# Kernel tuning notes

Measured on AMD Instinct MI355X. Metric: run time of the kernel, lower is better.

Reference implementation:

```python
import jax, jax.numpy as jnp
import numpy as np

B, D, H, NG = 8192, 2048, 2048, 7  # batch, input_size, hidden_size, num gate networks


def setup_inputs() -> dict:
    key = jax.random.key(0)
    ks = jax.random.split(key, 7)
    hx = jax.random.normal(ks[0], (B, D), dtype=jnp.float32)
    cx1 = jax.random.normal(ks[1], (B, H), dtype=jnp.float32)
    cx2 = jax.random.normal(ks[2], (B, H), dtype=jnp.float32)
    tj = jax.random.uniform(ks[3], (B, 1), dtype=jnp.float32)
    dt = jax.random.uniform(ks[4], (B, 1), dtype=jnp.float32)
    # fused weights for the 7 gate/decay networks, order: i1,i2,f1,f2,o,z,d
    W = jax.random.normal(ks[5], (D, NG * H), dtype=jnp.float32) * (1.0 / np.sqrt(D))
    b = jax.random.normal(ks[6], (NG * H,), dtype=jnp.float32) * 0.01
    return {"hx": hx, "cx1": cx1, "cx2": cx2, "tj": tj, "dt": dt, "W": W, "b": b}


def reference(hx, cx1, cx2, tj, dt, W, b):
    # One fused GEMM for all 7 gate networks, then split.
    g = hx @ W + b  # [B, 7H]
    i1, i2, f1, f2, o, z_raw, d_raw = [g[:, k * H:(k + 1) * H] for k in range(NG)]
    sig = jax.nn.sigmoid
    i1, i2, f1, f2, o = sig(i1), sig(i2), sig(f1), sig(f2), sig(o)
    z = jnp.tanh(z_raw)                 # Tanh(LC_z(hx)) as in forward
    decay = jax.nn.softplus(d_raw)      # Decay_network: positive decay coeff
    cy1 = f1 * cx1 + i1 * z             # fast cell state
    cy2 = f2 * cx2 + i2 * z             # asymptotic cell state
    t = tj + dt
    # continuous-time decay: c(t) = cy2 + (cy1 - cy2) * exp(-decay * (t - tj))
    c_t = cy2 + (cy1 - cy2) * jnp.exp(-decay * (t - tj))
    h_t = o * jnp.tanh(c_t)             # get_h(t)
    return jnp.stack([cy1, cy2, h_t])   # [3, B, H]
```

## Files before the change

### kernel.cpp

```cpp
#include <hip/hip_runtime.h>
#include <hip/hip_bf16.h>
#include <stdint.h>


#define B_SZ 8192
#define D_SZ 2048
#define H_SZ 2048
#define NG   7
#define NW   (NG * H_SZ)
#define BM   256
#define BK   64
#define NKT  (D_SZ / BK)
#define NBX  (B_SZ / BM)
#define NNB  (H_SZ / 32)

#define ATILE 32768
#define BTILE 28672
#define WB_BYTES   ((size_t)NNB * NKT * BTILE)
#define AB_OFF     WB_BYTES
#define AB_BYTES   ((size_t)NBX * NKT * ATILE)
#define WS_NEEDED  (WB_BYTES + AB_BYTES)

typedef __attribute__((ext_vector_type(8))) short bf16x8;
typedef __attribute__((ext_vector_type(4))) float f32x4;

__device__ __forceinline__ uint32_t cvtpk(float lo, float hi) {
    uint32_t r;
    asm("v_cvt_pk_bf16_f32 %0, %1, %2" : "=v"(r) : "v"(lo), "v"(hi));
    return r;
}
__device__ __forceinline__ void glds16(const void* g, void* l) {
    __builtin_amdgcn_global_load_lds(
        (const __attribute__((address_space(1))) uint32_t*)g,
        (__attribute__((address_space(3))) uint32_t*)l, 16, 0, 0);
}
__device__ __forceinline__ float sigmoidf_(float x) {
    return 1.0f / (1.0f + __expf(-x));
}
__device__ __forceinline__ float tanhf_(float x) {
    float ax = fabsf(x);
    float e = __expf(2.0f * ax);
    float t = 1.0f - 2.0f / (e + 1.0f);
    return copysignf(t, x);
}
__device__ __forceinline__ float softplusf_(float x) {
    return (x > 30.0f) ? x : __logf(1.0f + __expf(x));
}

__global__ __launch_bounds__(512) void conv_a(const float* __restrict__ hx,
                                              char* __restrict__ ai)
{
    const int bx = blockIdx.x >> 5;
    const int kt = blockIdx.x & 31;
    char* dst = ai + (size_t)(bx * NKT + kt) * ATILE;
    #pragma unroll
    for (int i = 0; i < 4; ++i) {
        int d = threadIdx.x + i * 512;
        int r = d >> 3, kq = d & 7;
        int koct = kq ^ ((r >> 1) & 3);
        const float* s = hx + (size_t)(bx * BM + r) * D_SZ + kt * BK + koct * 8;
        f32x4 a = *(const f32x4*)s;
        f32x4 b = *(const f32x4*)(s + 4);
        uint4 o;
        o.x = cvtpk(a[0], a[1]); o.y = cvtpk(a[2], a[3]);
        o.z = cvtpk(b[0], b[1]); o.w = cvtpk(b[2], b[3]);
        *(uint4*)(dst + d * 16) = o;
    }
}

__global__ __launch_bounds__(448) void conv_b(const float* __restrict__ W,
                                              char* __restrict__ bi)
{
    const int nb = blockIdx.x >> 5;
    const int kt = blockIdx.x & 31;
    char* dst = bi + (size_t)(nb * NKT + kt) * BTILE;
    const int cc = threadIdx.x % 224;
    const int kh = threadIdx.x / 224;
    const int q  = cc >> 4;
    const int gate = (q < 7) ? q : q - 7;
    const int hsub = ((q < 7) ? 0 : 16) + (cc & 15);
    const int n = gate * H_SZ + nb * 32 + hsub;
    #pragma unroll
    for (int i = 0; i < 4; ++i) {
        int kq = kh * 4 + i;
        int koct = kq ^ ((cc >> 1) & 3);
        const float* s = W + (size_t)(kt * BK + koct * 8) * NW + n;
        float w0 = s[0];
        float w1 = s[(size_t)NW];
        float w2 = s[(size_t)2 * NW];
        float w3 = s[(size_t)3 * NW];
        float w4 = s[(size_t)4 * NW];
        float w5 = s[(size_t)5 * NW];
        float w6 = s[(size_t)6 * NW];
        float w7 = s[(size_t)7 * NW];
        uint4 o;
        o.x = cvtpk(w0, w1); o.y = cvtpk(w2, w3);
        o.z = cvtpk(w4, w5); o.w = cvtpk(w6, w7);
        *(uint4*)(dst + cc * 128 + kq * 16) = o;
    }
}

#define MFMA_ __builtin_amdgcn_mfma_f32_16x16x32_bf16
#define SB0 __builtin_amdgcn_sched_barrier(0)
#define DSR(DST, BASE, OFF) \
    asm volatile("ds_read_b128 %0, %1 offset:" #OFF : "=v"(DST) : "v"(BASE));

__global__ __launch_bounds__(512, 2) void lstm_gemm(
    const char* __restrict__ bi, const char* __restrict__ ai,
    const float* __restrict__ cx1, const float* __restrict__ cx2,
    const float* __restrict__ dt, const float* __restrict__ bias,
    float* __restrict__ out)
{
    __shared__ char smem[2 * 61440];

    const int tid  = threadIdx.x;
    const int lane = tid & 63;
    const int wid  = tid >> 6;
    const int wm4  = wid >> 1;
    const int wn2  = wid & 1;
    const int l15  = lane & 15;
    const int lg   = lane >> 4;

    const int b0  = blockIdx.x;
    const int swz = (b0 & 7) * 256 + (b0 >> 3);
    const int bx  = swz >> 6;
    const int nb  = swz & 63;

    const int xch = lg ^ ((l15 >> 1) & 3);
    const uint32_t aA0 = (uint32_t)(uintptr_t)smem + wm4 * 8192 + l15 * 128 + xch * 16;
    const uint32_t aA1 = aA0 + 61440;
    const uint32_t aB0 = (uint32_t)(uintptr_t)smem + 32768 + wn2 * 14336 + l15 * 128 + xch * 16;
    const uint32_t aB1 = aB0 + 61440;

    char* dstA0 = smem + (wid << 12);
    char* dstA1 = dstA0 + 61440;
    char* dstB0 = smem + 32768 + wid * 3584;
    char* dstB1 = dstB0 + 61440;

    const char* qa = ai + (size_t)bx * (NKT * ATILE) + (wid << 12) + (lane << 4);
    const char* qb = bi + (size_t)nb * (NKT * BTILE) + wid * 3584 + (lane << 4);

    f32x4 acc[NG][4];
    #pragma unroll
    for (int g = 0; g < NG; ++g)
        #pragma unroll
        for (int mf = 0; mf < 4; ++mf)
            acc[g][mf] = (f32x4){0.f, 0.f, 0.f, 0.f};

    bf16x8 fA[4][2], fB0[2], fB1[2];

    #define RD_A(AA) \
        DSR(fA[0][0], AA, 0)    DSR(fA[0][1], AA, 64) \
        DSR(fA[1][0], AA, 2048) DSR(fA[1][1], AA, 2112) \
        DSR(fA[2][0], AA, 4096) DSR(fA[2][1], AA, 4160) \
        DSR(fA[3][0], AA, 6144) DSR(fA[3][1], AA, 6208)

    #define RD_B2(AB, O0, O1, O2, O3) \
        DSR(fB0[0], AB, O0) DSR(fB0[1], AB, O1) \
        DSR(fB1[0], AB, O2) DSR(fB1[1], AB, O3)

    #define PH_SYNC \
        SB0; __builtin_amdgcn_s_barrier(); \
        asm volatile("s_waitcnt lgkmcnt(0)" ::: "memory"); SB0;

    #define CL16(NA, NX) \
        __builtin_amdgcn_s_setprio(1); \
        _Pragma("unroll") \
        for (int mf_ = 0; mf_ < 4; ++mf_) { \
            acc[NA][mf_] = MFMA_(fA[mf_][0], fB0[0], acc[NA][mf_], 0, 0, 0); \
            acc[NA][mf_] = MFMA_(fA[mf_][1], fB0[1], acc[NA][mf_], 0, 0, 0); \
        } \
        _Pragma("unroll") \
        for (int mf_ = 0; mf_ < 4; ++mf_) { \
            acc[NX][mf_] = MFMA_(fA[mf_][0], fB1[0], acc[NX][mf_], 0, 0, 0); \
            acc[NX][mf_] = MFMA_(fA[mf_][1], fB1[1], acc[NX][mf_], 0, 0, 0); \
        } \
        __builtin_amdgcn_s_setprio(0); SB0;

    #define STG_A(NB_) do { \
        glds16(psA, dstA##NB_);            glds16(psA + 1024, dstA##NB_ + 1024); \
        glds16(psA + 2048, dstA##NB_ + 2048); glds16(psA + 3072, dstA##NB_ + 3072); \
        psA += ATILE; } while (0)

    #define STG_B(NB_) do { \
        glds16(psB, dstB##NB_);            glds16(psB + 1024, dstB##NB_ + 1024); \
        glds16(psB + 2048, dstB##NB_ + 2048); \
        if (lane < 32) glds16(psB + 3072, dstB##NB_ + 3072); \
        psB += BTILE; } while (0)

    #define TILE(B_, N_, STG) do { \
         \
        RD_A(aA##B_) \
        RD_B2(aB##B_, 0, 64, 2048, 2112) \
        if (STG) STG_A(N_); \
        PH_SYNC \
        CL16(0, 1) \
        __builtin_amdgcn_s_barrier(); \
         \
        RD_B2(aB##B_, 4096, 4160, 6144, 6208) \
        if (STG) STG_B(N_); \
        PH_SYNC \
        CL16(2, 3) \
        __builtin_amdgcn_s_barrier(); \
         \
        RD_B2(aB##B_, 8192, 8256, 10240, 10304) \
        PH_SYNC \
        CL16(4, 5) \
        __builtin_amdgcn_s_barrier(); \
         \
        DSR(fB0[0], aB##B_, 12288) DSR(fB0[1], aB##B_, 12352) \
        PH_SYNC \
        __builtin_amdgcn_s_setprio(1); \
        _Pragma("unroll") \
        for (int mf_ = 0; mf_ < 4; ++mf_) { \
            acc[6][mf_] = MFMA_(fA[mf_][0], fB0[0], acc[6][mf_], 0, 0, 0); \
            acc[6][mf_] = MFMA_(fA[mf_][1], fB0[1], acc[6][mf_], 0, 0, 0); \
        } \
        __builtin_amdgcn_s_setprio(0); SB0; \
        asm volatile("s_waitcnt vmcnt(0)" ::: "memory"); \
        __builtin_amdgcn_s_barrier(); \
        SB0; \
    } while (0)

    glds16(qa, dstA0);        glds16(qa + 1024, dstA0 + 1024);
    glds16(qa + 2048, dstA0 + 2048); glds16(qa + 3072, dstA0 + 3072);
    glds16(qb, dstB0);        glds16(qb + 1024, dstB0 + 1024);
    glds16(qb + 2048, dstB0 + 2048);
    if (lane < 32) glds16(qb + 3072, dstB0 + 3072);
    const char* psA = qa + ATILE;
    const char* psB = qb + BTILE;
    asm volatile("s_waitcnt vmcnt(0)" ::: "memory");
    __builtin_amdgcn_s_barrier();
    SB0;

    #pragma unroll 1
    for (int it = 0; it < 16; ++it) {
        TILE(0, 1, 1);
        TILE(1, 0, (it < 15));
    }

    const size_t BH = (size_t)B_SZ * H_SZ;
    const int h = nb * 32 + wn2 * 16 + l15;
    float bj[NG];
    #pragma unroll
    for (int g = 0; g < NG; ++g) bj[g] = bias[g * H_SZ + h];

    #pragma unroll
    for (int mf = 0; mf < 4; ++mf) {
        #pragma unroll
        for (int r = 0; r < 4; ++r) {
            int row = bx * BM + wm4 * 64 + mf * 16 + lg * 4 + r;
            float dtv = dt[row];
            float i1 = sigmoidf_(acc[0][mf][r] + bj[0]);
            float i2 = sigmoidf_(acc[1][mf][r] + bj[1]);
            float f1 = sigmoidf_(acc[2][mf][r] + bj[2]);
            float f2 = sigmoidf_(acc[3][mf][r] + bj[3]);
            float o  = sigmoidf_(acc[4][mf][r] + bj[4]);
            float z  = tanhf_(acc[5][mf][r] + bj[5]);
            float dec = softplusf_(acc[6][mf][r] + bj[6]);
            size_t idx = (size_t)row * H_SZ + h;
            float c1 = cx1[idx], c2 = cx2[idx];
            float cy1 = f1 * c1 + i1 * z;
            float cy2 = f2 * c2 + i2 * z;
            float ct  = cy2 + (cy1 - cy2) * __expf(-dec * dtv);
            float ht  = o * tanhf_(ct);
            out[idx]          = cy1;
            out[BH + idx]     = cy2;
            out[2 * BH + idx] = ht;
        }
    }
}

#define BN_  32
#define NTH  512
#define LDP  40
#define NKST 64
__global__ __launch_bounds__(NTH, 2) void lstm_f32(
    const float* __restrict__ hx, const float* __restrict__ cx1,
    const float* __restrict__ cx2, const float* __restrict__ dt,
    const float* __restrict__ W, const float* __restrict__ bias,
    float* __restrict__ out)
{
    __shared__ ushort sA[BM * LDP];
    __shared__ ushort sB[NG * BN_ * LDP];

    const int tid = threadIdx.x;
    const int nwg = gridDim.x;
    const int cpx = nwg >> 3;
    const int b0  = blockIdx.x;
    const int swz = (b0 & 7) * cpx + (b0 >> 3);
    const int bx  = swz & 31;
    const int by  = swz >> 5;
    const int gm0 = bx * BM;
    const int n0  = by * BN_;

    const int lane = tid & 63;
    const int wid  = tid >> 6;
    const int wm   = wid >> 1;
    const int wn   = wid & 1;
    const int l15  = lane & 15;
    const int lg   = lane >> 4;

    const int ar0 = tid >> 2,          aq0 = tid & 3;
    const int ar1 = (tid + 512) >> 2,  aq1 = tid & 3;
    const bool hasB = (tid < 448);
    const int bg  = tid >> 6;
    const int bkq = (tid >> 3) & 7;
    const int bnq = tid & 7;

    f32x4 pa[4];
    f32x4 pb[4];

    auto issue_loads = [&](int K0) {
        {
            const float* p = hx + (size_t)(gm0 + ar0) * D_SZ + K0 + aq0 * 8;
            pa[0] = *(const f32x4*)(p);
            pa[1] = *(const f32x4*)(p + 4);
        }
        {
            const float* p = hx + (size_t)(gm0 + ar1) * D_SZ + K0 + aq1 * 8;
            pa[2] = *(const f32x4*)(p);
            pa[3] = *(const f32x4*)(p + 4);
        }
        if (hasB) {
            const float* p = W + (size_t)(K0 + bkq * 4) * NW + bg * H_SZ + n0 + bnq * 4;
            pb[0] = *(const f32x4*)(p);
            pb[1] = *(const f32x4*)(p + NW);
            pb[2] = *(const f32x4*)(p + 2 * NW);
            pb[3] = *(const f32x4*)(p + 3 * NW);
        }
    };

    auto store_lds = [&]() {
        {
            uint4 u;
            u.x = cvtpk(pa[0][0], pa[0][1]); u.y = cvtpk(pa[0][2], pa[0][3]);
            u.z = cvtpk(pa[1][0], pa[1][1]); u.w = cvtpk(pa[1][2], pa[1][3]);
            *(uint4*)(&sA[ar0 * LDP + aq0 * 8]) = u;
        }
        {
            uint4 u;
            u.x = cvtpk(pa[2][0], pa[2][1]); u.y = cvtpk(pa[2][2], pa[2][3]);
            u.z = cvtpk(pa[3][0], pa[3][1]); u.w = cvtpk(pa[3][2], pa[3][3]);
            *(uint4*)(&sA[ar1 * LDP + aq1 * 8]) = u;
        }
        if (hasB) {
            #pragma unroll
            for (int jj = 0; jj < 4; ++jj) {
                uint2 v;
                v.x = cvtpk(pb[0][jj], pb[1][jj]);
                v.y = cvtpk(pb[2][jj], pb[3][jj]);
                *(uint2*)(&sB[(bg * BN_ + bnq * 4 + jj) * LDP + bkq * 4]) = v;
            }
        }
    };

    f32x4 acc[NG][4];
    #pragma unroll
    for (int g = 0; g < NG; ++g)
        #pragma unroll
        for (int mf = 0; mf < 4; ++mf)
            acc[g][mf] = (f32x4){0.f, 0.f, 0.f, 0.f};

    int aoff[4];
    #pragma unroll
    for (int mf = 0; mf < 4; ++mf)
        aoff[mf] = (wm * 64 + mf * 16 + l15) * LDP + lg * 8;
    int boff[NG];
    #pragma unroll
    for (int g = 0; g < NG; ++g)
        boff[g] = (g * BN_ + wn * 16 + l15) * LDP + lg * 8;

    issue_loads(0);
    for (int kk = 0; kk < NKST; ++kk) {
        store_lds();
        __syncthreads();
        if (kk + 1 < NKST) issue_loads((kk + 1) * 32);

        bf16x8 af[4];
        #pragma unroll
        for (int mf = 0; mf < 4; ++mf)
            af[mf] = *(const bf16x8*)(&sA[aoff[mf]]);
        #pragma unroll
        for (int g = 0; g < NG; ++g) {
            bf16x8 bfr = *(const bf16x8*)(&sB[boff[g]]);
            #pragma unroll
            for (int mf = 0; mf < 4; ++mf)
                acc[g][mf] = __builtin_amdgcn_mfma_f32_16x16x32_bf16(
                    af[mf], bfr, acc[g][mf], 0, 0, 0);
        }
        __syncthreads();
    }

    const size_t BH = (size_t)B_SZ * H_SZ;
    const int j = n0 + wn * 16 + l15;
    float bj[NG];
    #pragma unroll
    for (int g = 0; g < NG; ++g) bj[g] = bias[g * H_SZ + j];

    #pragma unroll
    for (int mf = 0; mf < 4; ++mf) {
        #pragma unroll
        for (int r = 0; r < 4; ++r) {
            int row = gm0 + wm * 64 + mf * 16 + lg * 4 + r;
            float dtv = dt[row];
            float i1 = sigmoidf_(acc[0][mf][r] + bj[0]);
            float i2 = sigmoidf_(acc[1][mf][r] + bj[1]);
            float f1 = sigmoidf_(acc[2][mf][r] + bj[2]);
            float f2 = sigmoidf_(acc[3][mf][r] + bj[3]);
            float o  = sigmoidf_(acc[4][mf][r] + bj[4]);
            float z  = tanhf_(acc[5][mf][r] + bj[5]);
            float dec = softplusf_(acc[6][mf][r] + bj[6]);
            size_t idx = (size_t)row * H_SZ + j;
            float c1 = cx1[idx], c2 = cx2[idx];
            float cy1 = f1 * c1 + i1 * z;
            float cy2 = f2 * c2 + i2 * z;
            float ct  = cy2 + (cy1 - cy2) * __expf(-dec * dtv);
            float ht  = o * tanhf_(ct);
            out[idx]          = cy1;
            out[BH + idx]     = cy2;
            out[2 * BH + idx] = ht;
        }
    }
}

extern "C" void kernel_launch(void* const* d_in, const int* in_sizes, int n_in,
                              void* d_out, int out_size, void* d_ws, size_t ws_size,
                              hipStream_t stream) {
    const float* hx  = (const float*)d_in[0];
    const float* cx1 = (const float*)d_in[1];
    const float* cx2 = (const float*)d_in[2];
    const float* dt  = (const float*)d_in[4];
    const float* W   = (const float*)d_in[5];
    const float* b   = (const float*)d_in[6];
    float* out = (float*)d_out;

    if (ws_size >= WS_NEEDED) {
        char* bimg = (char*)d_ws;
        char* aimg = (char*)d_ws + AB_OFF;
        conv_b<<<dim3(NNB * NKT), dim3(448), 0, stream>>>(W, bimg);
        conv_a<<<dim3(NBX * NKT), dim3(512), 0, stream>>>(hx, aimg);
        lstm_gemm<<<dim3(NBX * NNB), dim3(512), 0, stream>>>(
            bimg, aimg, cx1, cx2, dt, b, out);
    } else {
        lstm_f32<<<dim3(NBX * NNB / 2), dim3(NTH), 0, stream>>>(
            hx, cx1, cx2, dt, W, b, out);
    }
}
```

Baseline: 602.5 us.

## Split K tiles into 32-wide halves with finer-grained async LDS pipelining

Repacks the bf16 A and B images into two 32-wide K halves (64-byte rows) so each MFMA consumes one full fragment, and restructures the main loop to issue the loads for each half separately. Partial vmcnt waits replace the full drain at the end of each tile, so global-to-LDS copies overlap more with compute. The block-to-tile mapping is also changed so that pairs of N blocks share an A tile, aiming for better L2 reuse. The tradeoff is more barriers per tile and more intricate vmcnt bookkeeping, which risks races if the counts are wrong.

```diff
diff --git a/kernel.cpp b/kernel.cpp
--- a/kernel.cpp
+++ b/kernel.cpp
@@ -9,8 +9,7 @@
 #define NG   7
 #define NW   (NG * H_SZ)
 #define BM   256
-#define BK   64
-#define NKT  (D_SZ / BK)
+#define NKT  32
 #define NBX  (B_SZ / BM)
 #define NNB  (H_SZ / 32)
 
@@ -47,25 +46,22 @@
     return (x > 30.0f) ? x : __logf(1.0f + __expf(x));
 }
 
-__global__ __launch_bounds__(512) void conv_a(const float* __restrict__ hx,
-                                              char* __restrict__ ai)
+__global__ __launch_bounds__(1024) void conv_a(const float* __restrict__ hx,
+                                               char* __restrict__ ai)
 {
-    const int bx = blockIdx.x >> 5;
-    const int kt = blockIdx.x & 31;
-    char* dst = ai + (size_t)(bx * NKT + kt) * ATILE;
-    #pragma unroll
-    for (int i = 0; i < 4; ++i) {
-        int d = threadIdx.x + i * 512;
-        int r = d >> 3, kq = d & 7;
-        int koct = kq ^ ((r >> 1) & 3);
-        const float* s = hx + (size_t)(bx * BM + r) * D_SZ + kt * BK + koct * 8;
-        f32x4 a = *(const f32x4*)s;
-        f32x4 b = *(const f32x4*)(s + 4);
-        uint4 o;
-        o.x = cvtpk(a[0], a[1]); o.y = cvtpk(a[2], a[3]);
-        o.z = cvtpk(b[0], b[1]); o.w = cvtpk(b[2], b[3]);
-        *(uint4*)(dst + d * 16) = o;
-    }
+    const int bx = blockIdx.x >> 6;
+    const int ks = blockIdx.x & 63;
+    const int u  = threadIdx.x;
+    const int r  = u >> 2;
+    const int pc = u & 3;
+    const int koct = pc ^ ((r >> 1) & 3);
+    const float* src = hx + (size_t)(bx * BM + r) * D_SZ + ks * 32 + koct * 8;
+    f32x4 a = *(const f32x4*)(src);
+    f32x4 b = *(const f32x4*)(src + 4);
+    uint4 o;
+    o.x = cvtpk(a[0], a[1]); o.y = cvtpk(a[2], a[3]);
+    o.z = cvtpk(b[0], b[1]); o.w = cvtpk(b[2], b[3]);
+    *(uint4*)(ai + (size_t)blockIdx.x * 16384 + u * 16) = o;
 }
 
 __global__ __launch_bounds__(448) void conv_b(const float* __restrict__ W,
@@ -73,18 +69,18 @@
 {
     const int nb = blockIdx.x >> 5;
     const int kt = blockIdx.x & 31;
-    char* dst = bi + (size_t)(nb * NKT + kt) * BTILE;
+    char* dst = bi + (size_t)blockIdx.x * BTILE;
     const int cc = threadIdx.x % 224;
     const int kh = threadIdx.x / 224;
     const int q  = cc >> 4;
     const int gate = (q < 7) ? q : q - 7;
     const int hsub = ((q < 7) ? 0 : 16) + (cc & 15);
-    const int n = gate * H_SZ + nb * 32 + hsub;
-    #pragma unroll
-    for (int i = 0; i < 4; ++i) {
-        int kq = kh * 4 + i;
-        int koct = kq ^ ((cc >> 1) & 3);
-        const float* s = W + (size_t)(kt * BK + koct * 8) * NW + n;
+    const int n  = gate * H_SZ + nb * 32 + hsub;
+    const int xb = (cc >> 1) & 3;
+    #pragma unroll
+    for (int pc = 0; pc < 4; ++pc) {
+        const int k = kt * 64 + kh * 32 + (pc ^ xb) * 8;
+        const float* s = W + (size_t)k * NW + n;
         float w0 = s[0];
         float w1 = s[(size_t)NW];
         float w2 = s[(size_t)2 * NW];
@@ -96,7 +92,7 @@
         uint4 o;
         o.x = cvtpk(w0, w1); o.y = cvtpk(w2, w3);
         o.z = cvtpk(w4, w5); o.w = cvtpk(w6, w7);
-        *(uint4*)(dst + cc * 128 + kq * 16) = o;
+        *(uint4*)(dst + kh * 14336 + cc * 64 + pc * 16) = o;
     }
 }
 
@@ -123,22 +119,24 @@
 
     const int b0  = blockIdx.x;
     const int swz = (b0 & 7) * 256 + (b0 >> 3);
-    const int bx  = swz >> 6;
-    const int nb  = swz & 63;
+    const int nb2 = swz >> 6;
+    const int rem = swz & 63;
+    const int bx  = rem >> 1;
+    const int nb  = nb2 * 2 + (rem & 1);
 
     const int xch = lg ^ ((l15 >> 1) & 3);
-    const uint32_t aA0 = (uint32_t)(uintptr_t)smem + wm4 * 8192 + l15 * 128 + xch * 16;
-    const uint32_t aA1 = aA0 + 61440;
-    const uint32_t aB0 = (uint32_t)(uintptr_t)smem + 32768 + wn2 * 14336 + l15 * 128 + xch * 16;
-    const uint32_t aB1 = aB0 + 61440;
-
-    char* dstA0 = smem + (wid << 12);
-    char* dstA1 = dstA0 + 61440;
-    char* dstB0 = smem + 32768 + wid * 3584;
-    char* dstB1 = dstB0 + 61440;
-
-    const char* qa = ai + (size_t)bx * (NKT * ATILE) + (wid << 12) + (lane << 4);
-    const char* qb = bi + (size_t)nb * (NKT * BTILE) + wid * 3584 + (lane << 4);
+    const uint32_t aAb = (uint32_t)(uintptr_t)smem
+                       + (wm4 * 64 + l15) * 64 + xch * 16;
+    const uint32_t aBb = (uint32_t)(uintptr_t)smem + 32768
+                       + (wn2 * 112 + l15) * 64 + xch * 16;
+    const uint32_t aA0 = aAb, aA1 = aAb + 61440;
+    const uint32_t aB0 = aBb, aB1 = aBb + 61440;
+
+    const int lane16 = lane << 4;
+    const char* qa = ai + ((size_t)bx << 20) + (wid << 11) + lane16;
+    const char* qb = bi + (size_t)nb * (NKT * BTILE) + wid * 1792 + lane16;
+    char* dA0 = smem + (wid << 11);            char* dA1 = dA0 + 61440;
+    char* dB0 = smem + 32768 + wid * 1792;     char* dB1 = dB0 + 61440;
 
     f32x4 acc[NG][4];
     #pragma unroll
@@ -147,97 +145,84 @@
         for (int mf = 0; mf < 4; ++mf)
             acc[g][mf] = (f32x4){0.f, 0.f, 0.f, 0.f};
 
-    bf16x8 fA[4][2], fB0[2], fB1[2];
-
-    #define RD_A(AA) \
-        DSR(fA[0][0], AA, 0)    DSR(fA[0][1], AA, 64) \
-        DSR(fA[1][0], AA, 2048) DSR(fA[1][1], AA, 2112) \
-        DSR(fA[2][0], AA, 4096) DSR(fA[2][1], AA, 4160) \
-        DSR(fA[3][0], AA, 6144) DSR(fA[3][1], AA, 6208)
-
-    #define RD_B2(AB, O0, O1, O2, O3) \
-        DSR(fB0[0], AB, O0) DSR(fB0[1], AB, O1) \
-        DSR(fB1[0], AB, O2) DSR(fB1[1], AB, O3)
-
-    #define PH_SYNC \
-        SB0; __builtin_amdgcn_s_barrier(); \
-        asm volatile("s_waitcnt lgkmcnt(0)" ::: "memory"); SB0;
-
-    #define CL16(NA, NX) \
+    bf16x8 fA[4], fB[4];
+
+    #define CL16 \
         __builtin_amdgcn_s_setprio(1); \
         _Pragma("unroll") \
-        for (int mf_ = 0; mf_ < 4; ++mf_) { \
-            acc[NA][mf_] = MFMA_(fA[mf_][0], fB0[0], acc[NA][mf_], 0, 0, 0); \
-            acc[NA][mf_] = MFMA_(fA[mf_][1], fB0[1], acc[NA][mf_], 0, 0, 0); \
-        } \
+        for (int nf_ = 0; nf_ < 4; ++nf_) \
+            _Pragma("unroll") \
+            for (int mf_ = 0; mf_ < 4; ++mf_) \
+                acc[nf_][mf_] = MFMA_(fA[mf_], fB[nf_], acc[nf_][mf_], 0, 0, 0); \
+        __builtin_amdgcn_s_setprio(0); SB0;
+
+    #define CL12 \
+        __builtin_amdgcn_s_setprio(1); \
         _Pragma("unroll") \
-        for (int mf_ = 0; mf_ < 4; ++mf_) { \
-            acc[NX][mf_] = MFMA_(fA[mf_][0], fB1[0], acc[NX][mf_], 0, 0, 0); \
-            acc[NX][mf_] = MFMA_(fA[mf_][1], fB1[1], acc[NX][mf_], 0, 0, 0); \
-        } \
+        for (int nf_ = 0; nf_ < 3; ++nf_) \
+            _Pragma("unroll") \
+            for (int mf_ = 0; mf_ < 4; ++mf_) \
+                acc[4 + nf_][mf_] = MFMA_(fA[mf_], fB[nf_], acc[4 + nf_][mf_], 0, 0, 0); \
         __builtin_amdgcn_s_setprio(0); SB0;
 
-    #define STG_A(NB_) do { \
-        glds16(psA, dstA##NB_);            glds16(psA + 1024, dstA##NB_ + 1024); \
-        glds16(psA + 2048, dstA##NB_ + 2048); glds16(psA + 3072, dstA##NB_ + 3072); \
-        psA += ATILE; } while (0)
-
-    #define STG_B(NB_) do { \
-        glds16(psB, dstB##NB_);            glds16(psB + 1024, dstB##NB_ + 1024); \
-        glds16(psB + 2048, dstB##NB_ + 2048); \
-        if (lane < 32) glds16(psB + 3072, dstB##NB_ + 3072); \
-        psB += BTILE; } while (0)
-
-    #define TILE(B_, N_, STG) do { \
+    #define PH_SYNC \
+        SB0; \
+        __builtin_amdgcn_s_barrier(); \
+        asm volatile("s_waitcnt lgkmcnt(0)" ::: "memory"); SB0;
+
+    #define TILE(K, N, STG, VM2) do { \
          \
-        RD_A(aA##B_) \
-        RD_B2(aB##B_, 0, 64, 2048, 2112) \
-        if (STG) STG_A(N_); \
+        asm volatile("s_waitcnt vmcnt(4)" ::: "memory"); \
+        __builtin_amdgcn_s_barrier(); SB0; \
+        DSR(fA[0], aA##K, 0)     DSR(fA[1], aA##K, 1024) \
+        DSR(fA[2], aA##K, 2048)  DSR(fA[3], aA##K, 3072) \
+        DSR(fB[0], aB##K, 0)     DSR(fB[1], aB##K, 1024) \
+        DSR(fB[2], aB##K, 2048)  DSR(fB[3], aB##K, 3072) \
+        if (STG) { glds16(psA, dA##N); glds16(psA + 1024, dA##N + 1024); } \
         PH_SYNC \
-        CL16(0, 1) \
+        CL16 \
         __builtin_amdgcn_s_barrier(); \
          \
-        RD_B2(aB##B_, 4096, 4160, 6144, 6208) \
-        if (STG) STG_B(N_); \
+        DSR(fB[0], aB##K, 4096)  DSR(fB[1], aB##K, 5120)  DSR(fB[2], aB##K, 6144) \
+        if (STG) { glds16(psB, dB##N); if (lane < 48) glds16(psB + 1024, dB##N + 1024); } \
         PH_SYNC \
-        CL16(2, 3) \
+        CL12 \
+         \
+        asm volatile("s_waitcnt vmcnt(" #VM2 ")" ::: "memory"); \
+        __builtin_amdgcn_s_barrier(); SB0; \
+        DSR(fA[0], aA##K, 16384) DSR(fA[1], aA##K, 17408) \
+        DSR(fA[2], aA##K, 18432) DSR(fA[3], aA##K, 19456) \
+        DSR(fB[0], aB##K, 14336) DSR(fB[1], aB##K, 15360) \
+        DSR(fB[2], aB##K, 16384) DSR(fB[3], aB##K, 17408) \
+        if (STG) { glds16(psA + 16384, dA##N + 16384); \
+                   glds16(psA + 17408, dA##N + 17408); } \
+        PH_SYNC \
+        CL16 \
         __builtin_amdgcn_s_barrier(); \
          \
-        RD_B2(aB##B_, 8192, 8256, 10240, 10304) \
+        DSR(fB[0], aB##K, 18432) DSR(fB[1], aB##K, 19456) DSR(fB[2], aB##K, 20480) \
+        if (STG) { glds16(psB + 14336, dB##N + 14336); \
+                   if (lane < 48) glds16(psB + 15360, dB##N + 15360); \
+                   psA += ATILE; psB += BTILE; } \
         PH_SYNC \
-        CL16(4, 5) \
-        __builtin_amdgcn_s_barrier(); \
-         \
-        DSR(fB0[0], aB##B_, 12288) DSR(fB0[1], aB##B_, 12352) \
-        PH_SYNC \
-        __builtin_amdgcn_s_setprio(1); \
-        _Pragma("unroll") \
-        for (int mf_ = 0; mf_ < 4; ++mf_) { \
-            acc[6][mf_] = MFMA_(fA[mf_][0], fB0[0], acc[6][mf_], 0, 0, 0); \
-            acc[6][mf_] = MFMA_(fA[mf_][1], fB0[1], acc[6][mf_], 0, 0, 0); \
-        } \
-        __builtin_amdgcn_s_setprio(0); SB0; \
-        asm volatile("s_waitcnt vmcnt(0)" ::: "memory"); \
-        __builtin_amdgcn_s_barrier(); \
-        SB0; \
+        CL12 \
     } while (0)
 
-    glds16(qa, dstA0);        glds16(qa + 1024, dstA0 + 1024);
-    glds16(qa + 2048, dstA0 + 2048); glds16(qa + 3072, dstA0 + 3072);
-    glds16(qb, dstB0);        glds16(qb + 1024, dstB0 + 1024);
-    glds16(qb + 2048, dstB0 + 2048);
-    if (lane < 32) glds16(qb + 3072, dstB0 + 3072);
+    glds16(qa, dA0);           glds16(qa + 1024, dA0 + 1024);
+    glds16(qb, dB0);           if (lane < 48) glds16(qb + 1024, dB0 + 1024);
+    glds16(qa + 16384, dA0 + 16384); glds16(qa + 17408, dA0 + 17408);
+    glds16(qb + 14336, dB0 + 14336);
+    if (lane < 48) glds16(qb + 15360, dB0 + 15360);
     const char* psA = qa + ATILE;
     const char* psB = qb + BTILE;
-    asm volatile("s_waitcnt vmcnt(0)" ::: "memory");
-    __builtin_amdgcn_s_barrier();
-    SB0;
 
     #pragma unroll 1
-    for (int it = 0; it < 16; ++it) {
-        TILE(0, 1, 1);
-        TILE(1, 0, (it < 15));
-    }
+    for (int it = 0; it < 15; ++it) {
+        TILE(0, 1, 1, 4);
+        TILE(1, 0, 1, 4);
+    }
+    TILE(0, 1, 1, 4);
+    TILE(1, 0, 0, 0);
 
     const size_t BH = (size_t)B_SZ * H_SZ;
     const int h = nb * 32 + wn2 * 16 + l15;
@@ -439,7 +424,7 @@
         char* bimg = (char*)d_ws;
         char* aimg = (char*)d_ws + AB_OFF;
         conv_b<<<dim3(NNB * NKT), dim3(448), 0, stream>>>(W, bimg);
-        conv_a<<<dim3(NBX * NKT), dim3(512), 0, stream>>>(hx, aimg);
+        conv_a<<<dim3(NBX * 64), dim3(1024), 0, stream>>>(hx, aimg);
         lstm_gemm<<<dim3(NBX * NNB), dim3(512), 0, stream>>>(
             bimg, aimg, cx1, cx2, dt, b, out);
     } else {
```

Measured after the change: 564.6 us. 6.3% less time.
